# Kernel optimization log

Hardware: AMD Instinct MI355X
Metric: run time of the kernel (lower is better)

## Reference

```python
import jax, jax.numpy as jnp
import numpy as np


def conv1x1(x, w, b):
    # x: (B,C,H,W), w: (Cout,Cin), b: (Cout,) -- 1x1 conv == channel matmul
    return jnp.einsum('bchw,oc->bohw', x, w) + b[None, :, None, None]


def spatial_gate(q_feat, k_feat, scale):
    # Faithful to: matmul over flattened (B*HW, C) x (C, B*HW), then
    # max over keys, mean over the batch axis, softmax over spatial dims.
    B, C, H, W = q_feat.shape
    q = q_feat.reshape(B, C, H * W).transpose(0, 2, 1).reshape(B * H * W, C)
    k = k_feat.reshape(B, C, H * W).transpose(1, 0, 2).reshape(C, B * H * W)
    s = (q @ k).reshape(B * H * W, B, H * W)          # (BHW, B, HW)
    m = jnp.mean(jnp.max(s, axis=-1), axis=-1)        # (BHW,)
    w = jax.nn.softmax(m.reshape(B, H * W) * scale, axis=-1)
    return w.reshape(B, 1, H, W)


def setup_inputs() -> dict:
    key = jax.random.key(0)
    ks = jax.random.split(key, 10)
    C = 256
    shp = (8, C, 32, 32)
    inp = {
        'x4': jax.random.normal(ks[0], shp, jnp.float32),
        'x3': jax.random.normal(ks[1], shp, jnp.float32),
        'wq': jax.random.normal(ks[2], (C, C), jnp.float32) * 0.02,
        'bq': jnp.zeros((C,), jnp.float32),
        'wk': jax.random.normal(ks[3], (C, C), jnp.float32) * 0.02,
        'bk': jnp.zeros((C,), jnp.float32),
        'wv': jax.random.normal(ks[4], (C, C), jnp.float32) * 0.02,
        'bv': jnp.zeros((C,), jnp.float32),
        'w128': jax.random.normal(ks[5], (128, C), jnp.float32) * 0.02,
        'b128': jnp.zeros((128,), jnp.float32),
    }
    return inp


def reference(x4, x3, wq, bq, wk, bk, wv, bv, w128, b128):
    C = x4.shape[1]
    scale = 1.0 / (C ** 0.5)
    # shared QKV 1x1 convs applied to both inputs
    aq = conv1x1(x4, wq, bq)
    ak = conv1x1(x4, wk, bk)
    av = conv1x1(x4, wv, bv)
    bq_f = conv1x1(x3, wq, bq)
    bk_f = conv1x1(x3, wk, bk)
    bv_f = conv1x1(x3, wv, bv)
    # four gating branches: self-self (a), self-self (b), cross a->b, cross b->a
    a_x4 = conv1x1(spatial_gate(aq, ak, scale) * av, w128, b128)
    b_x3 = conv1x1(spatial_gate(bq_f, bk_f, scale) * bv_f, w128, b128)
    x43 = conv1x1(spatial_gate(aq, bk_f, scale) * bv_f, w128, b128)
    x34 = conv1x1(spatial_gate(bq_f, ak, scale) * av, w128, b128)
    # cat order: [x34, a_x4] then [x43, b_x3]
    ab_cat = jnp.concatenate([x34, a_x4, x43, b_x3], axis=1)  # (B,512,H,W)
    # Block2D loop: block class undefined in source; surrogate = identity
    # (ab12 = concat of the two chunks == ab_cat), applied depth=4 times.
    ab12 = ab_cat
    ab12 = ab_cat * ab12
    ab_avg = jnp.mean(ab12, axis=(2, 3), keepdims=True)        # (B,512,1,1)
    ab = jax.nn.softmax(ab_avg, axis=-1)   # softmax over size-1 axis -> ones
    final = ab * ab_cat
    return final
```

## Files before the change

### kernel.cpp

```cpp
#include <hip/hip_runtime.h>

typedef unsigned short ushort_t;
typedef unsigned char uchar_t;
typedef __attribute__((ext_vector_type(8))) short bf16x8;
typedef __attribute__((ext_vector_type(4))) float f32x4;
typedef __attribute__((ext_vector_type(16))) float f32x16;
typedef __attribute__((ext_vector_type(8))) int v8i;

__device__ __forceinline__ unsigned short f2bf(float f) {
  union { float f; unsigned int u; } v; v.f = f;
  unsigned int r = v.u + 0x7FFFu + ((v.u >> 16) & 1u);
  return (unsigned short)(r >> 16);
}

__device__ __forceinline__ float bf2f(unsigned short u) {
  union { unsigned int i; float f; } v; v.i = ((unsigned int)u) << 16;
  return v.f;
}

__device__ __forceinline__ void gl_lds16(const void* gsrc, void* ldst) {
  __builtin_amdgcn_global_load_lds(
      (const __attribute__((address_space(1))) void*)gsrc,
      (__attribute__((address_space(3))) void*)ldst, 16, 0, 0);
}

__device__ __forceinline__ int frag_idx(int oc, int ci) {
  return (((oc>>4)*8 + (ci>>5))<<9) + ((((ci>>3)&3)*16 + (oc&15))<<3) + (ci&7);
}

__global__ __launch_bounds__(256) void k1_weights(
    const float* __restrict__ wq, const float* __restrict__ bq,
    const float* __restrict__ wk, const float* __restrict__ bk,
    const float* __restrict__ wv, const float* __restrict__ bv,
    const float* __restrict__ w128,
    ushort_t* __restrict__ Wf, float* __restrict__ bias_all)
{
  const int ci = threadIdx.x;
  const int oc = blockIdx.x;
  if (oc < 512) {
    const float v = (oc < 256) ? wq[oc*256 + ci] : wk[(oc-256)*256 + ci];
    Wf[frag_idx(oc, ci)] = f2bf(v);
    if (ci == 0) bias_all[oc] = (oc < 256) ? bq[oc] : bk[oc-256];
  } else {
    const int o = oc - 512;
    const float* wr = w128 + (size_t)o*256;
    float a = 0.f;
    for (int co = 0; co < 256; co++) a += wr[co] * wv[co*256 + ci];
    Wf[frag_idx(oc, ci)] = f2bf(a);
    if (ci == 0) {
      float s = 0.f;
      for (int co = 0; co < 256; co++) s += wr[co] * bv[co];
      bias_all[oc] = s;
    }
  }
}

__global__ __launch_bounds__(256) void k2_features(
    const float* __restrict__ x4, const float* __restrict__ x3,
    const ushort_t* __restrict__ Wf, const float* __restrict__ bias_all,
    uchar_t* __restrict__ Qf8, uchar_t* __restrict__ Kf8, float* __restrict__ V)
{
  __shared__ ushort_t Af[32*512];
  __shared__ ushort_t Wl[2][32*512];
  __shared__ ushort_t Lt[64*72];

  const int tid = threadIdx.x;
  const int w = tid >> 6, lane = tid & 63;
  const int mrow = lane & 15, quad = lane >> 4;
  const int ln31 = lane & 31, half = lane >> 5;

  const int px0 = blockIdx.x * 64;
  const int src = px0 >> 13, b = (px0 >> 10) & 7, hw0 = px0 & 1023;
  const float* xp = (src ? x3 : x4) + (size_t)b*262144;

  const int ot0 = blockIdx.y * 5;

  for (int kb = 0; kb < 8; kb++)
    gl_lds16(Wf + ((size_t)((ot0*4 + w)*8 + kb)<<9) + lane*8,
             &Wl[ot0&1][(w*8+kb)*512]);

  {
    const int hw = hw0 + w*16 + mrow;
    for (int kb = 0; kb < 8; kb++) {
      const int ch0 = kb*32 + quad*8;
      bf16x8 pk;
      #pragma unroll
      for (int j = 0; j < 8; j++)
        ((ushort_t*)&pk)[j] = f2bf(xp[(size_t)(ch0 + j)*1024 + hw]);
      *(bf16x8*)&Af[(w*8 + kb)*512 + lane*8] = pk;
    }
  }
  __syncthreads();

  for (int ot = ot0; ot < ot0 + 5; ot++) {
    const int nbuf = (ot+1) & 1, cbuf = ot & 1;
    if (ot + 1 < ot0 + 5) {
      for (int kb = 0; kb < 8; kb++)
        gl_lds16(Wf + ((size_t)(((ot+1)*4 + w)*8 + kb)<<9) + lane*8,
                 &Wl[nbuf][(w*8+kb)*512]);
      asm volatile("s_waitcnt vmcnt(8)" ::: "memory");
    } else {
      asm volatile("s_waitcnt vmcnt(0)" ::: "memory");
    }

    f32x4 acc[4];
    #pragma unroll
    for (int lg = 0; lg < 4; lg++) acc[lg] = (f32x4){0.f,0.f,0.f,0.f};
    #pragma unroll
    for (int kb = 0; kb < 8; kb++) {
      const bf16x8 a = *(const bf16x8*)&Wl[cbuf][(w*8 + kb)*512 + lane*8];
      #pragma unroll
      for (int lg = 0; lg < 4; lg++) {
        const bf16x8 bx = *(const bf16x8*)&Af[(lg*8 + kb)*512 + lane*8];
        acc[lg] = __builtin_amdgcn_mfma_f32_16x16x32_bf16(a, bx, acc[lg], 0, 0, 0);
      }
    }
    const int ocl = w*16 + quad*4;
    const float4 bias4 = *(const float4*)&bias_all[ot*64 + ocl];

    if (ot < 8) {
      __syncthreads();
      #pragma unroll
      for (int lg = 0; lg < 4; lg++) {
        const int px = lg*16 + mrow;
        ushort4 pk;
        pk.x = f2bf(acc[lg][0] + bias4.x);
        pk.y = f2bf(acc[lg][1] + bias4.y);
        pk.z = f2bf(acc[lg][2] + bias4.z);
        pk.w = f2bf(acc[lg][3] + bias4.w);
        *(ushort4*)&Lt[px*72 + ocl] = pk;
      }
      __syncthreads();
      const int g = w >> 1, e = w & 1;
      const int row = g*32 + ln31;
      const ushort_t* lp = &Lt[row*72 + e*32 + half*8];
      float fl[8], fh[8];
      #pragma unroll
      for (int j = 0; j < 8; j++) { fl[j] = bf2f(lp[j]); fh[j] = bf2f(lp[16+j]); }
      int w0 = __builtin_amdgcn_cvt_pk_fp8_f32(fl[0], fl[1], 0, 0);
      w0     = __builtin_amdgcn_cvt_pk_fp8_f32(fl[2], fl[3], w0, 1);
      int w1 = __builtin_amdgcn_cvt_pk_fp8_f32(fl[4], fl[5], 0, 0);
      w1     = __builtin_amdgcn_cvt_pk_fp8_f32(fl[6], fl[7], w1, 1);
      int w2 = __builtin_amdgcn_cvt_pk_fp8_f32(fh[0], fh[1], 0, 0);
      w2     = __builtin_amdgcn_cvt_pk_fp8_f32(fh[2], fh[3], w2, 1);
      int w3 = __builtin_amdgcn_cvt_pk_fp8_f32(fh[4], fh[5], 0, 0);
      w3     = __builtin_amdgcn_cvt_pk_fp8_f32(fh[6], fh[7], w3, 1);
      uchar_t* dst = (ot < 4) ? Qf8 : Kf8;
      const size_t chunk = (size_t)((px0>>5) + g)*8 + (ot&3)*2 + e;
      int4 pk4; pk4.x = w0; pk4.y = w1; pk4.z = w2; pk4.w = w3;
      *(int4*)(dst + (chunk<<10) + lane*16) = pk4;
    } else {
      const int ocv0 = (ot-8)*64 + ocl;
      float* vb = V + (((size_t)(src*8 + b)*128) << 10) + hw0;
      #pragma unroll
      for (int lg = 0; lg < 4; lg++) {
        vb[(size_t)(ocv0+0)*1024 + lg*16 + mrow] = acc[lg][0] + bias4.x;
        vb[(size_t)(ocv0+1)*1024 + lg*16 + mrow] = acc[lg][1] + bias4.y;
        vb[(size_t)(ocv0+2)*1024 + lg*16 + mrow] = acc[lg][2] + bias4.z;
        vb[(size_t)(ocv0+3)*1024 + lg*16 + mrow] = acc[lg][3] + bias4.w;
      }
    }
  }
}

__global__ __launch_bounds__(256, 1) void k3_smax(
    const uchar_t* __restrict__ Qf8, const uchar_t* __restrict__ Kf8,
    float* __restrict__ Pm)
{
  __shared__ __align__(16) uchar_t Kl[2][32768];

  const int tid = threadIdx.x;
  const int bt = blockIdx.x >> 5;
  const int rt = blockIdx.x & 31;
  const int w = tid >> 6, lane = tid & 63;
  const int ln31 = lane & 31, half = lane >> 5;

  const int rgb = rt*16 + w*4;
  const int ph = (blockIdx.x & 1)*4;

  #pragma unroll
  for (int q = 0; q < 8; q++) {
    const int c = w*8 + q;
    const int cg = bt*32 + ph*4 + (c>>3);
    gl_lds16(Kf8 + (((size_t)cg*8 + (c&7))<<10) + lane*16, &Kl[0][c*1024]);
  }

  v8i qa[4][4];
  #pragma unroll
  for (int rg = 0; rg < 4; rg++)
    #pragma unroll
    for (int u = 0; u < 4; u++) {
      const int4 p0 = *(const int4*)(Qf8 + (((size_t)(rgb + rg)*8 + 2*u+0)<<10) + lane*16);
      const int4 p1 = *(const int4*)(Qf8 + (((size_t)(rgb + rg)*8 + 2*u+1)<<10) + lane*16);
      qa[rg][u] = (v8i){p0.x, p0.y, p0.z, p0.w, p1.x, p1.y, p1.z, p1.w};
    }

  f32x16 zv;
  #pragma unroll
  for (int i = 0; i < 16; i++) zv[i] = 0.f;
  f32x16 rmax[4];
  #pragma unroll
  for (int rg = 0; rg < 4; rg++)
    #pragma unroll
    for (int i = 0; i < 16; i++) rmax[rg][i] = -3.4e38f;

  for (int s = 0; s < 8; s++) {
    __syncthreads();
    if (s < 7) {
      const int sn = (s + 1 + ph) & 7;
      #pragma unroll
      for (int q = 0; q < 8; q++) {
        const int c = w*8 + q;
        const int cg = bt*32 + sn*4 + (c>>3);
        gl_lds16(Kf8 + (((size_t)cg*8 + (c&7))<<10) + lane*16,
                 &Kl[(s+1)&1][c*1024]);
      }
    }
    const uchar_t* kl = Kl[s & 1];
    #pragma unroll
    for (int cgl = 0; cgl < 4; cgl++) {
      f32x16 a0 = zv, a1 = zv, a2 = zv, a3 = zv;
      #pragma unroll
      for (int u = 0; u < 4; u++) {
        const int4 b0 = *(const int4*)&kl[(cgl*8 + 2*u+0)*1024 + lane*16];
        const int4 b1 = *(const int4*)&kl[(cgl*8 + 2*u+1)*1024 + lane*16];
        const v8i bu = (v8i){b0.x, b0.y, b0.z, b0.w, b1.x, b1.y, b1.z, b1.w};
        a0 = __builtin_amdgcn_mfma_scale_f32_32x32x64_f8f6f4(
            qa[0][u], bu, a0, 0, 0, 0, 0x7F7F7F7F, 0, 0x7F7F7F7F);
        a1 = __builtin_amdgcn_mfma_scale_f32_32x32x64_f8f6f4(
            qa[1][u], bu, a1, 0, 0, 0, 0x7F7F7F7F, 0, 0x7F7F7F7F);
        a2 = __builtin_amdgcn_mfma_scale_f32_32x32x64_f8f6f4(
            qa[2][u], bu, a2, 0, 0, 0, 0x7F7F7F7F, 0, 0x7F7F7F7F);
        a3 = __builtin_amdgcn_mfma_scale_f32_32x32x64_f8f6f4(
            qa[3][u], bu, a3, 0, 0, 0, 0x7F7F7F7F, 0, 0x7F7F7F7F);
      }
      #pragma unroll
      for (int i = 0; i < 16; i++) {
        rmax[0][i] = fmaxf(rmax[0][i], a0[i]);
        rmax[1][i] = fmaxf(rmax[1][i], a1[i]);
        rmax[2][i] = fmaxf(rmax[2][i], a2[i]);
        rmax[3][i] = fmaxf(rmax[3][i], a3[i]);
      }
    }
  }

  #pragma unroll
  for (int rg = 0; rg < 4; rg++) {
    #pragma unroll
    for (int e = 0; e < 16; e++) {
      float v = rmax[rg][e];
      v = fmaxf(v, __shfl_xor(v, 1));
      v = fmaxf(v, __shfl_xor(v, 2));
      v = fmaxf(v, __shfl_xor(v, 4));
      v = fmaxf(v, __shfl_xor(v, 8));
      v = fmaxf(v, __shfl_xor(v, 16));
      if (ln31 == 0) {
        const int row = rt*512 + w*128 + rg*32 + (e&3) + 8*(e>>2) + 4*half;
        Pm[(size_t)bt*16384 + row] = v;
      }
    }
  }
}

__global__ __launch_bounds__(256) void k5_out(
    const float* __restrict__ V, const float* __restrict__ Pm,
    const float* __restrict__ b128, float* __restrict__ out)
{
  __shared__ float xw[2][4];
  const int tid = threadIdx.x;
  const int ch = blockIdx.x & 511, b = blockIdx.x >> 9;
  const int blk = ch >> 7, o = ch & 127;
  const int gidx = (blk == 0) ? 2 : (blk == 1) ? 0 : (blk == 2) ? 1 : 3;
  const int src = (blk >= 2) ? 1 : 0;
  const int qset = gidx >> 1, side = gidx & 1;

  const float4* Pm4 = (const float4*)(Pm + (size_t)side*8*16384 + qset*8192 + b*1024);
  float4 l = {0.f, 0.f, 0.f, 0.f};
  #pragma unroll
  for (int t = 0; t < 8; t++) {
    const float4 p = Pm4[t*4096 + tid];
    l.x += p.x; l.y += p.y; l.z += p.z; l.w += p.w;
  }
  const float sc = 0.125f * 0.0625f;
  l.x *= sc; l.y *= sc; l.z *= sc; l.w *= sc;

  const int w = tid >> 6, lane = tid & 63;
  float m = fmaxf(fmaxf(l.x, l.y), fmaxf(l.z, l.w));
  #pragma unroll
  for (int d = 1; d < 64; d <<= 1) m = fmaxf(m, __shfl_xor(m, d));
  if (lane == 0) xw[0][w] = m;
  __syncthreads();
  m = fmaxf(fmaxf(xw[0][0], xw[0][1]), fmaxf(xw[0][2], xw[0][3]));

  float4 e;
  e.x = expf(l.x - m); e.y = expf(l.y - m);
  e.z = expf(l.z - m); e.w = expf(l.w - m);
  float s = e.x + e.y + e.z + e.w;
  #pragma unroll
  for (int d = 1; d < 64; d <<= 1) s += __shfl_xor(s, d);
  if (lane == 0) xw[1][w] = s;
  __syncthreads();
  s = xw[1][0] + xw[1][1] + xw[1][2] + xw[1][3];
  const float inv = 1.f / s;

  const int hw0 = tid << 2;
  const float4 v = *(const float4*)&V[((size_t)((src*8 + b)*128 + o) << 10) + hw0];
  const float bias = b128[o];
  float4 r;
  r.x = e.x*inv*v.x + bias; r.y = e.y*inv*v.y + bias;
  r.z = e.z*inv*v.z + bias; r.w = e.w*inv*v.w + bias;
  *(float4*)&out[((size_t)(b*512 + ch) << 10) + hw0] = r;
}

extern "C" void kernel_launch(void* const* d_in, const int* in_sizes, int n_in,
                              void* d_out, int out_size, void* d_ws, size_t ws_size,
                              hipStream_t stream)
{
  const float* x4   = (const float*)d_in[0];
  const float* x3   = (const float*)d_in[1];
  const float* wq   = (const float*)d_in[2];
  const float* bq   = (const float*)d_in[3];
  const float* wk   = (const float*)d_in[4];
  const float* bk   = (const float*)d_in[5];
  const float* wv   = (const float*)d_in[6];
  const float* bv   = (const float*)d_in[7];
  const float* w128 = (const float*)d_in[8];
  const float* b128 = (const float*)d_in[9];
  float* out = (float*)d_out;

  char* ws = (char*)d_ws;
  uchar_t*  Qf8 = (uchar_t*)ws;  ws += (size_t)512*8*1024;
  uchar_t*  Kf8 = (uchar_t*)ws;  ws += (size_t)512*8*1024;
  float*    V   = (float*)ws;    ws += (size_t)2*8*128*1024*4;
  float*    Pm  = (float*)ws;    ws += (size_t)16*16384*4;
  ushort_t* Wf  = (ushort_t*)ws; ws += (size_t)640*256*2;
  float* bias_all = (float*)ws;

  k1_weights <<<640,          256, 0, stream>>>(wq, bq, wk, bk, wv, bv, w128, Wf, bias_all);
  k2_features<<<dim3(256, 2), 256, 0, stream>>>(x4, x3, Wf, bias_all, Qf8, Kf8, V);
  k3_smax    <<<512,          256, 0, stream>>>(Qf8, Kf8, Pm);
  k5_out     <<<4096,         256, 0, stream>>>(V, Pm, b128, out);
}
```

Before: 200.3 us.

## Split k3_smax work across 8 waves with 2x2 MFMA register tiling

The max-reduction GEMM kernel goes from 4 to 8 waves per block, so each wave now covers 2 query row-groups instead of 4. This halves the Q fragment and running-max registers, allowing two blocks per CU. The inner loop becomes a 2x2 tile over two K column groups, so each pair of K LDS loads feeds four MFMAs. The cost is more LDS reads per MFMA, since each K fragment is now reused by 2 row-groups instead of 4.

```diff
diff --git a/kernel.cpp b/kernel.cpp
--- a/kernel.cpp
+++ b/kernel.cpp
@@ -163,7 +163,7 @@
   }
 }
 
-__global__ __launch_bounds__(256, 1) void k3_smax(
+__global__ __launch_bounds__(512, 2) void k3_smax(
     const uchar_t* __restrict__ Qf8, const uchar_t* __restrict__ Kf8,
     float* __restrict__ Pm)
 {
@@ -175,19 +175,19 @@
   const int w = tid >> 6, lane = tid & 63;
   const int ln31 = lane & 31, half = lane >> 5;
 
-  const int rgb = rt*16 + w*4;
+  const int rgb = rt*16 + w*2;
   const int ph = (blockIdx.x & 1)*4;
 
   #pragma unroll
-  for (int q = 0; q < 8; q++) {
-    const int c = w*8 + q;
+  for (int q = 0; q < 4; q++) {
+    const int c = w*4 + q;
     const int cg = bt*32 + ph*4 + (c>>3);
     gl_lds16(Kf8 + (((size_t)cg*8 + (c&7))<<10) + lane*16, &Kl[0][c*1024]);
   }
 
-  v8i qa[4][4];
-  #pragma unroll
-  for (int rg = 0; rg < 4; rg++)
+  v8i qa[2][4];
+  #pragma unroll
+  for (int rg = 0; rg < 2; rg++)
     #pragma unroll
     for (int u = 0; u < 4; u++) {
       const int4 p0 = *(const int4*)(Qf8 + (((size_t)(rgb + rg)*8 + 2*u+0)<<10) + lane*16);
@@ -198,9 +198,9 @@
   f32x16 zv;
   #pragma unroll
   for (int i = 0; i < 16; i++) zv[i] = 0.f;
-  f32x16 rmax[4];
-  #pragma unroll
-  for (int rg = 0; rg < 4; rg++)
+  f32x16 rmax[2];
+  #pragma unroll
+  for (int rg = 0; rg < 2; rg++)
     #pragma unroll
     for (int i = 0; i < 16; i++) rmax[rg][i] = -3.4e38f;
 
@@ -209,8 +209,8 @@
     if (s < 7) {
       const int sn = (s + 1 + ph) & 7;
       #pragma unroll
-      for (int q = 0; q < 8; q++) {
-        const int c = w*8 + q;
+      for (int q = 0; q < 4; q++) {
+        const int c = w*4 + q;
         const int cg = bt*32 + sn*4 + (c>>3);
         gl_lds16(Kf8 + (((size_t)cg*8 + (c&7))<<10) + lane*16,
                  &Kl[(s+1)&1][c*1024]);
@@ -218,34 +218,36 @@
     }
     const uchar_t* kl = Kl[s & 1];
     #pragma unroll
-    for (int cgl = 0; cgl < 4; cgl++) {
-      f32x16 a0 = zv, a1 = zv, a2 = zv, a3 = zv;
+    for (int cgp = 0; cgp < 2; cgp++) {
+      const int cA = 2*cgp, cB = 2*cgp + 1;
+      f32x16 a00 = zv, a01 = zv, a10 = zv, a11 = zv;
       #pragma unroll
       for (int u = 0; u < 4; u++) {
-        const int4 b0 = *(const int4*)&kl[(cgl*8 + 2*u+0)*1024 + lane*16];
-        const int4 b1 = *(const int4*)&kl[(cgl*8 + 2*u+1)*1024 + lane*16];
-        const v8i bu = (v8i){b0.x, b0.y, b0.z, b0.w, b1.x, b1.y, b1.z, b1.w};
-        a0 = __builtin_amdgcn_mfma_scale_f32_32x32x64_f8f6f4(
-            qa[0][u], bu, a0, 0, 0, 0, 0x7F7F7F7F, 0, 0x7F7F7F7F);
-        a1 = __builtin_amdgcn_mfma_scale_f32_32x32x64_f8f6f4(
-            qa[1][u], bu, a1, 0, 0, 0, 0x7F7F7F7F, 0, 0x7F7F7F7F);
-        a2 = __builtin_amdgcn_mfma_scale_f32_32x32x64_f8f6f4(
-            qa[2][u], bu, a2, 0, 0, 0, 0x7F7F7F7F, 0, 0x7F7F7F7F);
-        a3 = __builtin_amdgcn_mfma_scale_f32_32x32x64_f8f6f4(
-            qa[3][u], bu, a3, 0, 0, 0, 0x7F7F7F7F, 0, 0x7F7F7F7F);
+        const int4 b0 = *(const int4*)&kl[(cA*8 + 2*u+0)*1024 + lane*16];
+        const int4 b1 = *(const int4*)&kl[(cA*8 + 2*u+1)*1024 + lane*16];
+        const v8i buA = (v8i){b0.x, b0.y, b0.z, b0.w, b1.x, b1.y, b1.z, b1.w};
+        const int4 c0 = *(const int4*)&kl[(cB*8 + 2*u+0)*1024 + lane*16];
+        const int4 c1 = *(const int4*)&kl[(cB*8 + 2*u+1)*1024 + lane*16];
+        const v8i buB = (v8i){c0.x, c0.y, c0.z, c0.w, c1.x, c1.y, c1.z, c1.w};
+        a00 = __builtin_amdgcn_mfma_scale_f32_32x32x64_f8f6f4(
+            qa[0][u], buA, a00, 0, 0, 0, 0x7F7F7F7F, 0, 0x7F7F7F7F);
+        a10 = __builtin_amdgcn_mfma_scale_f32_32x32x64_f8f6f4(
+            qa[1][u], buA, a10, 0, 0, 0, 0x7F7F7F7F, 0, 0x7F7F7F7F);
+        a01 = __builtin_amdgcn_mfma_scale_f32_32x32x64_f8f6f4(
+            qa[0][u], buB, a01, 0, 0, 0, 0x7F7F7F7F, 0, 0x7F7F7F7F);
+        a11 = __builtin_amdgcn_mfma_scale_f32_32x32x64_f8f6f4(
+            qa[1][u], buB, a11, 0, 0, 0, 0x7F7F7F7F, 0, 0x7F7F7F7F);
       }
       #pragma unroll
       for (int i = 0; i < 16; i++) {
-        rmax[0][i] = fmaxf(rmax[0][i], a0[i]);
-        rmax[1][i] = fmaxf(rmax[1][i], a1[i]);
-        rmax[2][i] = fmaxf(rmax[2][i], a2[i]);
-        rmax[3][i] = fmaxf(rmax[3][i], a3[i]);
-      }
-    }
-  }
-
-  #pragma unroll
-  for (int rg = 0; rg < 4; rg++) {
+        rmax[0][i] = fmaxf(fmaxf(a00[i], a01[i]), rmax[0][i]);
+        rmax[1][i] = fmaxf(fmaxf(a10[i], a11[i]), rmax[1][i]);
+      }
+    }
+  }
+
+  #pragma unroll
+  for (int rg = 0; rg < 2; rg++) {
     #pragma unroll
     for (int e = 0; e < 16; e++) {
       float v = rmax[rg][e];
@@ -255,7 +257,7 @@
       v = fmaxf(v, __shfl_xor(v, 8));
       v = fmaxf(v, __shfl_xor(v, 16));
       if (ln31 == 0) {
-        const int row = rt*512 + w*128 + rg*32 + (e&3) + 8*(e>>2) + 4*half;
+        const int row = rt*512 + w*64 + rg*32 + (e&3) + 8*(e>>2) + 4*half;
         Pm[(size_t)bt*16384 + row] = v;
       }
     }
@@ -338,6 +340,6 @@
 
   k1_weights <<<640,          256, 0, stream>>>(wq, bq, wk, bk, wv, bv, w128, Wf, bias_all);
   k2_features<<<dim3(256, 2), 256, 0, stream>>>(x4, x3, Wf, bias_all, Qf8, Kf8, V);
-  k3_smax    <<<512,          256, 0, stream>>>(Qf8, Kf8, Pm);
+  k3_smax    <<<512,          512, 0, stream>>>(Qf8, Kf8, Pm);
   k5_out     <<<4096,         256, 0, stream>>>(V, Pm, b128, out);
 }
```

After: 195.6 us. -2.4%, faster.
